# Kernel tuning notes

Measured on AMD Instinct MI355X. Metric: run time of the kernel, lower is better.

## Reference

```python
import jax, jax.numpy as jnp
import numpy as np

B, S, T = 256, 1024, 64  # batch, seq_len, num_tags


def setup_inputs() -> dict:
    key = jax.random.key(0)
    k1, k2, k3 = jax.random.split(key, 3)
    emissions = jax.random.normal(k1, (B, S, T), dtype=jnp.float32)
    tags = jax.random.randint(k2, (B, S), 0, T)
    mask = jnp.ones((B, S), dtype=bool)
    # nn.init.normal_(transitions, mean=0, std=0.1)
    transitions = 0.1 * jax.random.normal(k3, (T, T), dtype=jnp.float32)
    return {"emissions": emissions, "tags": tags, "mask": mask, "transitions": transitions}


def _crf_nll(emissions, transitions, tags, mask):
    maskf = mask.astype(emissions.dtype)
    # ---- gold score (_score_sentence) ----
    emit = jnp.take_along_axis(emissions, tags[..., None], axis=2)[..., 0]  # [B,S]
    emit_scores = (emit * maskf).sum(axis=1)
    trans_scores = (transitions[tags[:, :-1], tags[:, 1:]] * maskf[:, 1:]).sum(axis=1)
    gold = emit_scores + trans_scores  # [B]

    # ---- partition function (_forward_alg) via lax.scan ----
    alpha0 = emissions[:, 0]                      # [B,T]
    em_t = jnp.swapaxes(emissions[:, 1:], 0, 1)   # [S-1,B,T] time-major
    mk_t = jnp.swapaxes(mask[:, 1:], 0, 1)        # [S-1,B]

    def step(alpha, xs):
        e, m = xs
        # scores[b,i,j] = alpha[b,i] + trans[i,j] + emit[b,j]
        scores = alpha[:, :, None] + transitions[None, :, :] + e[:, None, :]
        new_alpha = jax.nn.logsumexp(scores, axis=1)  # [B,T]
        return jnp.where(m[:, None], new_alpha, alpha), None

    alpha, _ = jax.lax.scan(step, alpha0, (em_t, mk_t))
    fwd_score = jax.nn.logsumexp(alpha, axis=1)  # [B]

    # reduction='mean'
    return (fwd_score - gold).mean()


def reference(emissions, tags, mask, transitions):
    return _crf_nll(emissions, transitions, tags, mask)
```

## Files before the change

kernel.cpp:

```cpp
#include <hip/hip_runtime.h>
#include <hip/hip_bf16.h>
#include <cstdint>
#include <cstddef>


#define BB 256
#define SS 1024
#define TT 64
#define LN2f 0.69314718055994530942f

typedef _Float16 h2  __attribute__((ext_vector_type(2)));
typedef _Float16 h8  __attribute__((ext_vector_type(8)));
typedef float    f32x16 __attribute__((ext_vector_type(16)));
typedef int      i4v __attribute__((ext_vector_type(4)));

__device__ __forceinline__ float wred(float v) {
#pragma unroll
    for (int m = 32; m; m >>= 1) v += __shfl_xor(v, m, 64);
    return v;
}

__device__ __forceinline__ float rescale(float qn, int& kacc) {
    int bq = __builtin_amdgcn_readfirstlane(__float_as_int(qn));
    int k  = ((bq >> 23) & 255) - 127;
    kacc += k;
    return qn * __int_as_float((127 - k) << 23);
}

__device__ __forceinline__ float matvec64(float bc, const h2* Epk) {
    int nq = __builtin_amdgcn_mov_dpp(__float_as_int(bc), 0xB1, 0xF, 0xF, true);
    int pki = __builtin_bit_cast(int,
                  __builtin_amdgcn_cvt_pkrtz(bc, __int_as_float(nq)));
    int sp[32];
#pragma unroll
    for (int p = 0; p < 32; ++p)
        sp[p] = __builtin_amdgcn_readlane(pki, 2 * p);
    float a0 = 0.f, a1 = 0.f, a2 = 0.f, a3 = 0.f;
#pragma unroll
    for (int p = 0; p < 32; p += 4) {
        a0 = __builtin_amdgcn_fdot2(__builtin_bit_cast(h2, sp[p + 0]), Epk[p + 0], a0, false);
        a1 = __builtin_amdgcn_fdot2(__builtin_bit_cast(h2, sp[p + 1]), Epk[p + 1], a1, false);
        a2 = __builtin_amdgcn_fdot2(__builtin_bit_cast(h2, sp[p + 2]), Epk[p + 2], a2, false);
        a3 = __builtin_amdgcn_fdot2(__builtin_bit_cast(h2, sp[p + 3]), Epk[p + 3], a3, false);
    }
    return (a0 + a1) + (a2 + a3);
}

#define VSTEPF(EVAL)                                                       \
    {                                                                      \
        float ee = __expf(EVAL);                                           \
        float t  = matvec64(state, Epk);                                   \
        state    = rescale(t * ee, kacc);                                  \
    }
#define VSTEPB(EVAL)                                                       \
    {                                                                      \
        float ee = __expf(EVAL);                                           \
        float t  = matvec64(state * ee, Epk);                              \
        state    = rescale(t, kacc);                                       \
    }

#define PKRTZ(a, b) __builtin_bit_cast(int, __builtin_amdgcn_cvt_pkrtz((a), (b)))
#define SWAP32(x, y) asm("v_permlane32_swap_b32 %0, %1" : "+v"(x), "+v"(y))

#define CONV(CC, OUTA, OUTB)                                               \
    {                                                                      \
        int p0 = PKRTZ(CC[0], CC[1]);   int p1 = PKRTZ(CC[2], CC[3]);      \
        int p2 = PKRTZ(CC[4], CC[5]);   int p3 = PKRTZ(CC[6], CC[7]);      \
        SWAP32(p0, p2);  SWAP32(p1, p3);                                   \
        i4v da = {p0, p1, p2, p3};                                         \
        OUTA = __builtin_bit_cast(h8, da);                                 \
        int q0 = PKRTZ(CC[8], CC[9]);   int q1 = PKRTZ(CC[10], CC[11]);    \
        int q2 = PKRTZ(CC[12], CC[13]); int q3 = PKRTZ(CC[14], CC[15]);    \
        SWAP32(q0, q2);  SWAP32(q1, q3);                                   \
        i4v db = {q0, q1, q2, q3};                                         \
        OUTB = __builtin_bit_cast(h8, db);                                 \
    }

__device__ __forceinline__ f32x16 zz16() {
    f32x16 z;
#pragma unroll
    for (int q = 0; q < 16; ++q) z[q] = 0.f;
    return z;
}

#define MSTEP(E0V, E1V)                                                    \
    {                                                                      \
        float ee0 = __expf(E0V), ee1 = __expf(E1V);                        \
        float m0f = ee0 * minv, m1f = ee1 * minv;                          \
        h2 mp0 = __builtin_bit_cast(h2, __builtin_amdgcn_cvt_pkrtz(m0f, m0f)); \
        h2 mp1 = __builtin_bit_cast(h2, __builtin_amdgcn_cvt_pkrtz(m1f, m1f)); \
        h8 ms0 = __builtin_shufflevector(mp0, mp0, 0,1,0,1,0,1,0,1);       \
        h8 ms1 = __builtin_shufflevector(mp1, mp1, 0,1,0,1,0,1,0,1);       \
        h8 A0[4], A1[4];                                                   \
        _Pragma("unroll")                                                  \
        for (int kk = 0; kk < 4; ++kk) { A0[kk] = EfT[0][kk] * ms0;        \
                                         A1[kk] = EfT[1][kk] * ms1; }      \
        f32x16 c00 = zz16(), c01 = zz16(), c10 = zz16(), c11 = zz16();     \
        _Pragma("unroll")                                                  \
        for (int kk = 0; kk < 4; ++kk) {                                   \
            c00 = __builtin_amdgcn_mfma_f32_32x32x16_f16(A0[kk], Mb[0][kk], c00, 0, 0, 0); \
            c01 = __builtin_amdgcn_mfma_f32_32x32x16_f16(A0[kk], Mb[1][kk], c01, 0, 0, 0); \
            c10 = __builtin_amdgcn_mfma_f32_32x32x16_f16(A1[kk], Mb[0][kk], c10, 0, 0, 0); \
            c11 = __builtin_amdgcn_mfma_f32_32x32x16_f16(A1[kk], Mb[1][kk], c11, 0, 0, 0); \
        }                                                                  \
        int bq = __builtin_amdgcn_readfirstlane(__float_as_int(c00[0]));   \
        int k  = ((bq >> 23) & 255) - 127;                                 \
        kacc += k;                                                         \
        minv = __int_as_float((127 - k) << 23);                            \
        CONV(c00, Mb[0][0], Mb[0][1]);                                     \
        CONV(c10, Mb[0][2], Mb[0][3]);                                     \
        CONV(c01, Mb[1][0], Mb[1][1]);                                     \
        CONV(c11, Mb[1][2], Mb[1][3]);                                     \
    }

__device__ __forceinline__ void gold_gather(const float* __restrict__ em,
                                            const float* __restrict__ trans,
                                            const int* t0v, const int* t1v,
                                            int w, int j,
                                            float* ge, float* gt) {
#pragma unroll
    for (int c = 0; c < 4; ++c) {
        int s = (w * 4 + c) * TT + j;
        ge[c] = em[s * TT + t0v[c]];
        float tr = trans[t0v[c] * TT + t1v[c]];
        gt[c] = (s == SS - 1) ? 0.f : tr;
    }
}

__global__ __launch_bounds__(256) void crf_fwd_kernel(
    const float* __restrict__ emissions,
    const int*   __restrict__ tags,
    const float* __restrict__ trans,
    float*       __restrict__ ws)
{
    const int b   = blockIdx.x;
    const int tid = threadIdx.x;
    const int w   = tid >> 6;
    const int j   = tid & 63;
    const float* em = emissions + (size_t)b * (SS * TT);
    const int*   tg = tags + b * SS;

    __shared__ float shq[TT];
    __shared__ float shr[TT];
    __shared__ float shu[TT];
    __shared__ float shM[2][TT][65];
    __shared__ float shg[4];
    __shared__ int   shk_[4];

    int t0v[4], t1v[4];
#pragma unroll
    for (int c = 0; c < 4; ++c) {
        int s = (w * 4 + c) * TT + j;
        t0v[c] = tg[s];
        t1v[c] = tg[(s < SS - 1) ? s + 1 : s];
    }

    float ge[4], gt[4];
    int   kacc = 0;

    if (w < 2) {
        h2 Epk[32];
        float state;
        if (w == 0) {
#pragma unroll
            for (int p = 0; p < 32; ++p) {
                float x = __expf(trans[(2 * p + 0) * TT + j]);
                float y = __expf(trans[(2 * p + 1) * TT + j]);
                Epk[p] = __builtin_bit_cast(h2, __builtin_amdgcn_cvt_pkrtz(x, y));
            }
            state = __expf(em[j]);
            float eb[8];
#pragma unroll
            for (int u = 0; u < 8; ++u) eb[u] = em[(1 + u) * TT + j];
            gold_gather(em, trans, t0v, t1v, w, j, ge, gt);
            for (int s0 = 1; s0 < 264; s0 += 8) {
                float en[8];
#pragma unroll
                for (int u = 0; u < 8; ++u)
                    en[u] = em[(s0 + 8 + u) * TT + j];
#pragma unroll
                for (int u = 0; u < 8; ++u) VSTEPF(eb[u]);
#pragma unroll
                for (int u = 0; u < 8; ++u) eb[u] = en[u];
            }
            shq[j] = state;
        } else {
#pragma unroll
            for (int p = 0; p < 32; ++p) {
                float x = __expf(trans[j * TT + 2 * p + 0]);
                float y = __expf(trans[j * TT + 2 * p + 1]);
                Epk[p] = __builtin_bit_cast(h2, __builtin_amdgcn_cvt_pkrtz(x, y));
            }
            state = 1.0f;
            float ep[7], eb[8];
#pragma unroll
            for (int u = 0; u < 7; ++u) ep[u] = em[(1023 - u) * TT + j];
#pragma unroll
            for (int u = 0; u < 8; ++u) eb[u] = em[(1016 - u) * TT + j];
            gold_gather(em, trans, t0v, t1v, w, j, ge, gt);
#pragma unroll
            for (int u = 0; u < 7; ++u) VSTEPB(ep[u]);
            for (int t0 = 0; t0 < 256; t0 += 8) {
                float en[8];
#pragma unroll
                for (int u = 0; u < 8; ++u)
                    en[u] = em[(1016 - (t0 + 8 + u)) * TT + j];
#pragma unroll
                for (int u = 0; u < 8; ++u) VSTEPB(eb[u]);
#pragma unroll
                for (int u = 0; u < 8; ++u) eb[u] = en[u];
            }
            shr[j] = state;
        }
    } else {
        const int hh  = j >> 5;
        const int cc_ = j & 31;
        const int sbeg = (w == 2) ? 265 : 513;

        h8 EfT[2][4];
#pragma unroll
        for (int rr = 0; rr < 2; ++rr)
#pragma unroll
            for (int kk = 0; kk < 4; ++kk) {
                h8 v;
#pragma unroll
                for (int e = 0; e < 8; ++e)
                    v[e] = (_Float16)__expf(trans[(16 * kk + 8 * hh + e) * TT + 32 * rr + cc_]);
                EfT[rr][kk] = v;
            }
        h8 Mb[2][4];
#pragma unroll
        for (int gg = 0; gg < 2; ++gg)
#pragma unroll
            for (int kk = 0; kk < 4; ++kk) {
                h8 v;
#pragma unroll
                for (int e = 0; e < 8; ++e)
                    v[e] = (_Float16)((16 * kk + 8 * hh + e == 32 * gg + cc_) ? 1.0f : 0.0f);
                Mb[gg][kk] = v;
            }

        float minv = 1.0f;
        float eb0[4], eb1[4];
#pragma unroll
        for (int u = 0; u < 4; ++u) {
            eb0[u] = em[(sbeg + u) * TT + cc_];
            eb1[u] = em[(sbeg + u) * TT + 32 + cc_];
        }
        gold_gather(em, trans, t0v, t1v, w, j, ge, gt);

        for (int s0 = 0; s0 < 248; s0 += 4) {
            float en0[4], en1[4];
#pragma unroll
            for (int u = 0; u < 4; ++u) {
                en0[u] = em[(sbeg + s0 + 4 + u) * TT + cc_];
                en1[u] = em[(sbeg + s0 + 4 + u) * TT + 32 + cc_];
            }
#pragma unroll
            for (int u = 0; u < 4; ++u) MSTEP(eb0[u], eb1[u]);
#pragma unroll
            for (int u = 0; u < 4; ++u) { eb0[u] = en0[u]; eb1[u] = en1[u]; }
        }

        float* shMp = &shM[w - 2][0][0];
#pragma unroll
        for (int gg = 0; gg < 2; ++gg)
#pragma unroll
            for (int kk = 0; kk < 4; ++kk)
#pragma unroll
                for (int e = 0; e < 8; ++e)
                    shMp[(16 * kk + 8 * hh + e) * 65 + 32 * gg + cc_] =
                        (float)Mb[gg][kk][e] * minv;
    }

    float g = 0.f;
#pragma unroll
    for (int c = 0; c < 4; ++c) g += ge[c] + gt[c];
    g = wred(g);
    if (j == 0) { shg[w] = g; shk_[w] = kacc; }
    __syncthreads();

    if (w == 0) {
        float u_ = 0.f;
#pragma unroll 8
        for (int i = 0; i < TT; ++i) u_ += shq[i] * shM[0][j][i];
        shu[j] = u_;
        float y = 0.f;
#pragma unroll 8
        for (int i = 0; i < TT; ++i) y += shu[i] * shM[1][j][i];
        float pr  = y * shr[j];
        float sum = wred(pr);
        float fwd = __logf(sum) +
                    (float)(shk_[0] + shk_[1] + shk_[2] + shk_[3]) * LN2f;
        if (j == 0) ws[b] = fwd - (shg[0] + shg[1] + shg[2] + shg[3]);
    }
}

__global__ __launch_bounds__(256) void crf_reduce_kernel(
    const float* __restrict__ ws, float* __restrict__ out)
{
    int t = threadIdx.x;
    float v = ws[t];
#pragma unroll
    for (int m = 32; m; m >>= 1) v += __shfl_xor(v, m, 64);
    __shared__ float sh[4];
    if ((t & 63) == 0) sh[t >> 6] = v;
    __syncthreads();
    if (t == 0) out[0] = (sh[0] + sh[1] + sh[2] + sh[3]) * (1.0f / BB);
}

extern "C" void kernel_launch(void* const* d_in, const int* in_sizes, int n_in,
                              void* d_out, int out_size, void* d_ws, size_t ws_size,
                              hipStream_t stream) {
    const float* emissions = (const float*)d_in[0];
    const int*   tags      = (const int*)d_in[1];
    const float* trans     = (const float*)d_in[3];
    float* ws = (float*)d_ws;

    crf_fwd_kernel<<<BB, 256, 0, stream>>>(emissions, tags, trans, ws);
    crf_reduce_kernel<<<1, BB, 0, stream>>>(ws, (float*)d_out);
}
```

Before: 205.5 us.

## Split CRF sequence scan across six waves with four MFMA matrix segments

Raises the block from four waves to six. The two vector waves now scan longer forward and backward segments, and four MFMA waves each build a transfer-matrix product over a shorter 108-step middle chunk, so the serial dependency chain per wave gets shorter. Segment matrices are stored in fp16 shared memory without the last rescale factor. The combine step chains four matrix-vector products instead of two. The first MFMA of each step now takes a zero constant directly instead of a zeroed accumulator. Risks include more registers per block, lower occupancy, extra serial combine work and fp16 precision loss in the stored matrices.

```diff
diff --git a/kernel.cpp b/kernel.cpp
--- a/kernel.cpp
+++ b/kernel.cpp
@@ -8,6 +8,10 @@
 #define SS 1024
 #define TT 64
 #define LN2f 0.69314718055994530942f
+#define VF 296
+#define VB 295
+#define MM 108
+#define SB1 297
 
 typedef _Float16 h2  __attribute__((ext_vector_type(2)));
 typedef _Float16 h8  __attribute__((ext_vector_type(8)));
@@ -95,9 +99,12 @@
         _Pragma("unroll")                                                  \
         for (int kk = 0; kk < 4; ++kk) { A0[kk] = EfT[0][kk] * ms0;        \
                                          A1[kk] = EfT[1][kk] * ms1; }      \
-        f32x16 c00 = zz16(), c01 = zz16(), c10 = zz16(), c11 = zz16();     \
+        f32x16 c00 = __builtin_amdgcn_mfma_f32_32x32x16_f16(A0[0], Mb[0][0], CZ, 0, 0, 0); \
+        f32x16 c01 = __builtin_amdgcn_mfma_f32_32x32x16_f16(A0[0], Mb[1][0], CZ, 0, 0, 0); \
+        f32x16 c10 = __builtin_amdgcn_mfma_f32_32x32x16_f16(A1[0], Mb[0][0], CZ, 0, 0, 0); \
+        f32x16 c11 = __builtin_amdgcn_mfma_f32_32x32x16_f16(A1[0], Mb[1][0], CZ, 0, 0, 0); \
         _Pragma("unroll")                                                  \
-        for (int kk = 0; kk < 4; ++kk) {                                   \
+        for (int kk = 1; kk < 4; ++kk) {                                   \
             c00 = __builtin_amdgcn_mfma_f32_32x32x16_f16(A0[kk], Mb[0][kk], c00, 0, 0, 0); \
             c01 = __builtin_amdgcn_mfma_f32_32x32x16_f16(A0[kk], Mb[1][kk], c01, 0, 0, 0); \
             c10 = __builtin_amdgcn_mfma_f32_32x32x16_f16(A1[kk], Mb[0][kk], c10, 0, 0, 0); \
@@ -105,7 +112,7 @@
         }                                                                  \
         int bq = __builtin_amdgcn_readfirstlane(__float_as_int(c00[0]));   \
         int k  = ((bq >> 23) & 255) - 127;                                 \
-        kacc += k;                                                         \
+        kacc += k;  klast = k;                                             \
         minv = __int_as_float((127 - k) << 23);                            \
         CONV(c00, Mb[0][0], Mb[0][1]);                                     \
         CONV(c10, Mb[0][2], Mb[0][3]);                                     \
@@ -116,18 +123,18 @@
 __device__ __forceinline__ void gold_gather(const float* __restrict__ em,
                                             const float* __restrict__ trans,
                                             const int* t0v, const int* t1v,
-                                            int w, int j,
+                                            int qw, int j,
                                             float* ge, float* gt) {
 #pragma unroll
     for (int c = 0; c < 4; ++c) {
-        int s = (w * 4 + c) * TT + j;
+        int s = (qw * 4 + c) * TT + j;
         ge[c] = em[s * TT + t0v[c]];
         float tr = trans[t0v[c] * TT + t1v[c]];
         gt[c] = (s == SS - 1) ? 0.f : tr;
     }
 }
 
-__global__ __launch_bounds__(256) void crf_fwd_kernel(
+__global__ __launch_bounds__(384) void crf_fwd_kernel(
     const float* __restrict__ emissions,
     const int*   __restrict__ tags,
     const float* __restrict__ trans,
@@ -140,82 +147,86 @@
     const float* em = emissions + (size_t)b * (SS * TT);
     const int*   tg = tags + b * SS;
 
-    __shared__ float shq[TT];
-    __shared__ float shr[TT];
-    __shared__ float shu[TT];
-    __shared__ float shM[2][TT][65];
-    __shared__ float shg[4];
-    __shared__ int   shk_[4];
+    __shared__ float     shq[TT];
+    __shared__ float     shr[TT];
+    __shared__ float     shu[TT];
+    __shared__ _Float16  shM[4][TT][66];
+    __shared__ float     shg[6];
+    __shared__ int       shk_[6];
 
     int t0v[4], t1v[4];
-#pragma unroll
-    for (int c = 0; c < 4; ++c) {
-        int s = (w * 4 + c) * TT + j;
-        t0v[c] = tg[s];
-        t1v[c] = tg[(s < SS - 1) ? s + 1 : s];
-    }
-
-    float ge[4], gt[4];
+    if (w < 4) {
+#pragma unroll
+        for (int c = 0; c < 4; ++c) {
+            int s = (w * 4 + c) * TT + j;
+            t0v[c] = tg[s];
+            t1v[c] = tg[(s < SS - 1) ? s + 1 : s];
+        }
+    }
+
+    float ge[4] = {0.f, 0.f, 0.f, 0.f}, gt[4] = {0.f, 0.f, 0.f, 0.f};
     int   kacc = 0;
-
-    if (w < 2) {
+    int   krep = 0;
+
+    if (w == 2) {
         h2 Epk[32];
-        float state;
-        if (w == 0) {
-#pragma unroll
-            for (int p = 0; p < 32; ++p) {
-                float x = __expf(trans[(2 * p + 0) * TT + j]);
-                float y = __expf(trans[(2 * p + 1) * TT + j]);
-                Epk[p] = __builtin_bit_cast(h2, __builtin_amdgcn_cvt_pkrtz(x, y));
-            }
-            state = __expf(em[j]);
-            float eb[8];
-#pragma unroll
-            for (int u = 0; u < 8; ++u) eb[u] = em[(1 + u) * TT + j];
-            gold_gather(em, trans, t0v, t1v, w, j, ge, gt);
-            for (int s0 = 1; s0 < 264; s0 += 8) {
-                float en[8];
-#pragma unroll
-                for (int u = 0; u < 8; ++u)
-                    en[u] = em[(s0 + 8 + u) * TT + j];
-#pragma unroll
-                for (int u = 0; u < 8; ++u) VSTEPF(eb[u]);
-#pragma unroll
-                for (int u = 0; u < 8; ++u) eb[u] = en[u];
-            }
-            shq[j] = state;
-        } else {
-#pragma unroll
-            for (int p = 0; p < 32; ++p) {
-                float x = __expf(trans[j * TT + 2 * p + 0]);
-                float y = __expf(trans[j * TT + 2 * p + 1]);
-                Epk[p] = __builtin_bit_cast(h2, __builtin_amdgcn_cvt_pkrtz(x, y));
-            }
-            state = 1.0f;
-            float ep[7], eb[8];
-#pragma unroll
-            for (int u = 0; u < 7; ++u) ep[u] = em[(1023 - u) * TT + j];
-#pragma unroll
-            for (int u = 0; u < 8; ++u) eb[u] = em[(1016 - u) * TT + j];
-            gold_gather(em, trans, t0v, t1v, w, j, ge, gt);
-#pragma unroll
-            for (int u = 0; u < 7; ++u) VSTEPB(ep[u]);
-            for (int t0 = 0; t0 < 256; t0 += 8) {
-                float en[8];
-#pragma unroll
-                for (int u = 0; u < 8; ++u)
-                    en[u] = em[(1016 - (t0 + 8 + u)) * TT + j];
-#pragma unroll
-                for (int u = 0; u < 8; ++u) VSTEPB(eb[u]);
-#pragma unroll
-                for (int u = 0; u < 8; ++u) eb[u] = en[u];
-            }
-            shr[j] = state;
-        }
+#pragma unroll
+        for (int p = 0; p < 32; ++p) {
+            float x = __expf(trans[(2 * p + 0) * TT + j]);
+            float y = __expf(trans[(2 * p + 1) * TT + j]);
+            Epk[p] = __builtin_bit_cast(h2, __builtin_amdgcn_cvt_pkrtz(x, y));
+        }
+        float state = __expf(em[j]);
+        float eb[8];
+#pragma unroll
+        for (int u = 0; u < 8; ++u) eb[u] = em[(1 + u) * TT + j];
+        gold_gather(em, trans, t0v, t1v, w, j, ge, gt);
+        for (int s0 = 1; s0 < 1 + VF; s0 += 8) {
+            float en[8];
+#pragma unroll
+            for (int u = 0; u < 8; ++u)
+                en[u] = em[(s0 + 8 + u) * TT + j];
+#pragma unroll
+            for (int u = 0; u < 8; ++u) VSTEPF(eb[u]);
+#pragma unroll
+            for (int u = 0; u < 8; ++u) eb[u] = en[u];
+        }
+        shq[j] = state;
+        krep = kacc;
+    } else if (w == 3) {
+        h2 Epk[32];
+#pragma unroll
+        for (int p = 0; p < 32; ++p) {
+            float x = __expf(trans[j * TT + 2 * p + 0]);
+            float y = __expf(trans[j * TT + 2 * p + 1]);
+            Epk[p] = __builtin_bit_cast(h2, __builtin_amdgcn_cvt_pkrtz(x, y));
+        }
+        float state = 1.0f;
+        float ep[7], eb[8];
+#pragma unroll
+        for (int u = 0; u < 7; ++u) ep[u] = em[(1023 - u) * TT + j];
+#pragma unroll
+        for (int u = 0; u < 8; ++u) eb[u] = em[(1016 - u) * TT + j];
+        gold_gather(em, trans, t0v, t1v, w, j, ge, gt);
+#pragma unroll
+        for (int u = 0; u < 7; ++u) VSTEPB(ep[u]);
+        for (int t0 = 0; t0 < 288; t0 += 8) {
+            float en[8];
+#pragma unroll
+            for (int u = 0; u < 8; ++u)
+                en[u] = em[(1016 - (t0 + 8 + u)) * TT + j];
+#pragma unroll
+            for (int u = 0; u < 8; ++u) VSTEPB(eb[u]);
+#pragma unroll
+            for (int u = 0; u < 8; ++u) eb[u] = en[u];
+        }
+        shr[j] = state;
+        krep = kacc;
     } else {
-        const int hh  = j >> 5;
-        const int cc_ = j & 31;
-        const int sbeg = (w == 2) ? 265 : 513;
+        const int mi   = (w < 2) ? w : (w - 2);
+        const int sbeg = SB1 + MM * mi;
+        const int hh   = j >> 5;
+        const int cc_  = j & 31;
 
         h8 EfT[2][4];
 #pragma unroll
@@ -240,16 +251,18 @@
                 Mb[gg][kk] = v;
             }
 
+        const f32x16 CZ = zz16();
         float minv = 1.0f;
+        int   klast = 0;
         float eb0[4], eb1[4];
 #pragma unroll
         for (int u = 0; u < 4; ++u) {
             eb0[u] = em[(sbeg + u) * TT + cc_];
             eb1[u] = em[(sbeg + u) * TT + 32 + cc_];
         }
-        gold_gather(em, trans, t0v, t1v, w, j, ge, gt);
-
-        for (int s0 = 0; s0 < 248; s0 += 4) {
+        if (w < 4) gold_gather(em, trans, t0v, t1v, w, j, ge, gt);
+
+        for (int s0 = 0; s0 < MM; s0 += 4) {
             float en0[4], en1[4];
 #pragma unroll
             for (int u = 0; u < 4; ++u) {
@@ -262,37 +275,41 @@
             for (int u = 0; u < 4; ++u) { eb0[u] = en0[u]; eb1[u] = en1[u]; }
         }
 
-        float* shMp = &shM[w - 2][0][0];
 #pragma unroll
         for (int gg = 0; gg < 2; ++gg)
 #pragma unroll
             for (int kk = 0; kk < 4; ++kk)
 #pragma unroll
                 for (int e = 0; e < 8; ++e)
-                    shMp[(16 * kk + 8 * hh + e) * 65 + 32 * gg + cc_] =
-                        (float)Mb[gg][kk][e] * minv;
+                    shM[mi][16 * kk + 8 * hh + e][32 * gg + cc_] = Mb[gg][kk][e];
+        krep = kacc - klast;
     }
 
     float g = 0.f;
 #pragma unroll
     for (int c = 0; c < 4; ++c) g += ge[c] + gt[c];
     g = wred(g);
-    if (j == 0) { shg[w] = g; shk_[w] = kacc; }
+    if (j == 0) { shg[w] = g; shk_[w] = krep; }
     __syncthreads();
 
-    if (w == 0) {
-        float u_ = 0.f;
+    if (w == 2) {
+        float uv = 0.f;
 #pragma unroll 8
-        for (int i = 0; i < TT; ++i) u_ += shq[i] * shM[0][j][i];
-        shu[j] = u_;
-        float y = 0.f;
+        for (int i = 0; i < TT; ++i) uv += shq[i] * (float)shM[0][j][i];
+#pragma unroll 1
+        for (int m = 1; m < 4; ++m) {
+            shu[j] = uv;
+            float acc = 0.f;
 #pragma unroll 8
-        for (int i = 0; i < TT; ++i) y += shu[i] * shM[1][j][i];
-        float pr  = y * shr[j];
+            for (int i = 0; i < TT; ++i) acc += shu[i] * (float)shM[m][j][i];
+            uv = acc;
+        }
+        float pr  = uv * shr[j];
         float sum = wred(pr);
-        float fwd = __logf(sum) +
-                    (float)(shk_[0] + shk_[1] + shk_[2] + shk_[3]) * LN2f;
-        if (j == 0) ws[b] = fwd - (shg[0] + shg[1] + shg[2] + shg[3]);
+        int ksum = shk_[0] + shk_[1] + shk_[2] + shk_[3] + shk_[4] + shk_[5];
+        float fwd = __logf(sum) + (float)ksum * LN2f;
+        float gsum = shg[0] + shg[1] + shg[2] + shg[3] + shg[4] + shg[5];
+        if (j == 0) ws[b] = fwd - gsum;
     }
 }
 
@@ -317,6 +334,6 @@
     const float* trans     = (const float*)d_in[3];
     float* ws = (float*)d_ws;
 
-    crf_fwd_kernel<<<BB, 256, 0, stream>>>(emissions, tags, trans, ws);
+    crf_fwd_kernel<<<BB, 384, 0, stream>>>(emissions, tags, trans, ws);
     crf_reduce_kernel<<<1, BB, 0, stream>>>(ws, (float*)d_out);
 }
```

After: 165.8 us. -19.3%, faster.

## Split CRF sequence across six waves with interleaved matrix chains and backward matrix-vector combine

Applied to the files above, without the earlier changes.

Each block grows from four to six waves. Two waves now run the forward and backward vector recurrences over about 272 steps each. Four MFMA waves each run two independent 60-step transfer-matrix chains, interleaved so their latencies overlap. The matrix products are applied to the backward vector in sequence, with exponent rescaling, through shared memory instead of storing full fp32 matrices. The gold-score gather moves onto the vector waves. This shortens the serial critical path per sequence at the cost of more waves per block, more registers, and eight synchronized combine steps at the end.

```diff
diff --git a/kernel.cpp b/kernel.cpp
--- a/kernel.cpp
+++ b/kernel.cpp
@@ -8,6 +8,10 @@
 #define SS 1024
 #define TT 64
 #define LN2f 0.69314718055994530942f
+#define VF 272
+#define VB 271
+#define MMs 60
+#define MSB 273
 
 typedef _Float16 h2  __attribute__((ext_vector_type(2)));
 typedef _Float16 h8  __attribute__((ext_vector_type(8)));
@@ -83,10 +87,10 @@
     return z;
 }
 
-#define MSTEP(E0V, E1V)                                                    \
+#define MSTEP(MB, MINV, KACC, KLAST, E0V, E1V)                             \
     {                                                                      \
         float ee0 = __expf(E0V), ee1 = __expf(E1V);                        \
-        float m0f = ee0 * minv, m1f = ee1 * minv;                          \
+        float m0f = ee0 * MINV, m1f = ee1 * MINV;                          \
         h2 mp0 = __builtin_bit_cast(h2, __builtin_amdgcn_cvt_pkrtz(m0f, m0f)); \
         h2 mp1 = __builtin_bit_cast(h2, __builtin_amdgcn_cvt_pkrtz(m1f, m1f)); \
         h8 ms0 = __builtin_shufflevector(mp0, mp0, 0,1,0,1,0,1,0,1);       \
@@ -95,39 +99,28 @@
         _Pragma("unroll")                                                  \
         for (int kk = 0; kk < 4; ++kk) { A0[kk] = EfT[0][kk] * ms0;        \
                                          A1[kk] = EfT[1][kk] * ms1; }      \
-        f32x16 c00 = zz16(), c01 = zz16(), c10 = zz16(), c11 = zz16();     \
+        f32x16 c00 = __builtin_amdgcn_mfma_f32_32x32x16_f16(A0[0], MB[0][0], CZ, 0, 0, 0); \
+        f32x16 c01 = __builtin_amdgcn_mfma_f32_32x32x16_f16(A0[0], MB[1][0], CZ, 0, 0, 0); \
+        f32x16 c10 = __builtin_amdgcn_mfma_f32_32x32x16_f16(A1[0], MB[0][0], CZ, 0, 0, 0); \
+        f32x16 c11 = __builtin_amdgcn_mfma_f32_32x32x16_f16(A1[0], MB[1][0], CZ, 0, 0, 0); \
         _Pragma("unroll")                                                  \
-        for (int kk = 0; kk < 4; ++kk) {                                   \
-            c00 = __builtin_amdgcn_mfma_f32_32x32x16_f16(A0[kk], Mb[0][kk], c00, 0, 0, 0); \
-            c01 = __builtin_amdgcn_mfma_f32_32x32x16_f16(A0[kk], Mb[1][kk], c01, 0, 0, 0); \
-            c10 = __builtin_amdgcn_mfma_f32_32x32x16_f16(A1[kk], Mb[0][kk], c10, 0, 0, 0); \
-            c11 = __builtin_amdgcn_mfma_f32_32x32x16_f16(A1[kk], Mb[1][kk], c11, 0, 0, 0); \
+        for (int kk = 1; kk < 4; ++kk) {                                   \
+            c00 = __builtin_amdgcn_mfma_f32_32x32x16_f16(A0[kk], MB[0][kk], c00, 0, 0, 0); \
+            c01 = __builtin_amdgcn_mfma_f32_32x32x16_f16(A0[kk], MB[1][kk], c01, 0, 0, 0); \
+            c10 = __builtin_amdgcn_mfma_f32_32x32x16_f16(A1[kk], MB[0][kk], c10, 0, 0, 0); \
+            c11 = __builtin_amdgcn_mfma_f32_32x32x16_f16(A1[kk], MB[1][kk], c11, 0, 0, 0); \
         }                                                                  \
         int bq = __builtin_amdgcn_readfirstlane(__float_as_int(c00[0]));   \
         int k  = ((bq >> 23) & 255) - 127;                                 \
-        kacc += k;                                                         \
-        minv = __int_as_float((127 - k) << 23);                            \
-        CONV(c00, Mb[0][0], Mb[0][1]);                                     \
-        CONV(c10, Mb[0][2], Mb[0][3]);                                     \
-        CONV(c01, Mb[1][0], Mb[1][1]);                                     \
-        CONV(c11, Mb[1][2], Mb[1][3]);                                     \
-    }
-
-__device__ __forceinline__ void gold_gather(const float* __restrict__ em,
-                                            const float* __restrict__ trans,
-                                            const int* t0v, const int* t1v,
-                                            int w, int j,
-                                            float* ge, float* gt) {
-#pragma unroll
-    for (int c = 0; c < 4; ++c) {
-        int s = (w * 4 + c) * TT + j;
-        ge[c] = em[s * TT + t0v[c]];
-        float tr = trans[t0v[c] * TT + t1v[c]];
-        gt[c] = (s == SS - 1) ? 0.f : tr;
-    }
-}
-
-__global__ __launch_bounds__(256) void crf_fwd_kernel(
+        KACC += k;  KLAST = k;                                             \
+        MINV = __int_as_float((127 - k) << 23);                            \
+        CONV(c00, MB[0][0], MB[0][1]);                                     \
+        CONV(c10, MB[0][2], MB[0][3]);                                     \
+        CONV(c01, MB[1][0], MB[1][1]);                                     \
+        CONV(c11, MB[1][2], MB[1][3]);                                     \
+    }
+
+__global__ __launch_bounds__(384) void crf_fwd_kernel(
     const float* __restrict__ emissions,
     const int*   __restrict__ tags,
     const float* __restrict__ trans,
@@ -141,27 +134,35 @@
     const int*   tg = tags + b * SS;
 
     __shared__ float shq[TT];
-    __shared__ float shr[TT];
     __shared__ float shu[TT];
-    __shared__ float shM[2][TT][65];
-    __shared__ float shg[4];
-    __shared__ int   shk_[4];
-
-    int t0v[4], t1v[4];
-#pragma unroll
-    for (int c = 0; c < 4; ++c) {
-        int s = (w * 4 + c) * TT + j;
-        t0v[c] = tg[s];
-        t1v[c] = tg[(s < SS - 1) ? s + 1 : s];
-    }
-
-    float ge[4], gt[4];
-    int   kacc = 0;
-
-    if (w < 2) {
+    __shared__ float shg[2];
+    __shared__ int   shkk[10];
+    __shared__ int   shkr;
+
+    if (tid == 0) shkr = 0;
+
+    const bool isMat = (w == 0) || (w == 1) || (w == 4) || (w == 5);
+    const int  widx  = (w < 2) ? w : (w - 2);
+    const int  hh    = j >> 5;
+    const int  cc_   = j & 31;
+
+    h8 MbA[2][4], MbB[2][4];
+
+    if (w == 2 || w == 3) {
+        int t0v[8], t1v[8];
+#pragma unroll
+        for (int c = 0; c < 8; ++c) {
+            int s = ((w - 2) * 8 + c) * TT + j;
+            t0v[c] = tg[s];
+            t1v[c] = tg[(s < SS - 1) ? s + 1 : s];
+        }
+
         h2 Epk[32];
         float state;
-        if (w == 0) {
+        int  kacc = 0;
+        float ge[8], gt[8];
+
+        if (w == 2) {
 #pragma unroll
             for (int p = 0; p < 32; ++p) {
                 float x = __expf(trans[(2 * p + 0) * TT + j]);
@@ -172,8 +173,13 @@
             float eb[8];
 #pragma unroll
             for (int u = 0; u < 8; ++u) eb[u] = em[(1 + u) * TT + j];
-            gold_gather(em, trans, t0v, t1v, w, j, ge, gt);
-            for (int s0 = 1; s0 < 264; s0 += 8) {
+#pragma unroll
+            for (int c = 0; c < 8; ++c) {
+                int s = (0 * 8 + c) * TT + j;
+                ge[c] = em[s * TT + t0v[c]];
+                gt[c] = trans[t0v[c] * TT + t1v[c]];
+            }
+            for (int s0 = 1; s0 < 1 + VF; s0 += 8) {
                 float en[8];
 #pragma unroll
                 for (int u = 0; u < 8; ++u)
@@ -197,10 +203,16 @@
             for (int u = 0; u < 7; ++u) ep[u] = em[(1023 - u) * TT + j];
 #pragma unroll
             for (int u = 0; u < 8; ++u) eb[u] = em[(1016 - u) * TT + j];
-            gold_gather(em, trans, t0v, t1v, w, j, ge, gt);
+#pragma unroll
+            for (int c = 0; c < 8; ++c) {
+                int s = (8 + c) * TT + j;
+                ge[c] = em[s * TT + t0v[c]];
+                float tr = trans[t0v[c] * TT + t1v[c]];
+                gt[c] = (s == SS - 1) ? 0.f : tr;
+            }
 #pragma unroll
             for (int u = 0; u < 7; ++u) VSTEPB(ep[u]);
-            for (int t0 = 0; t0 < 256; t0 += 8) {
+            for (int t0 = 0; t0 < VB - 7; t0 += 8) {
                 float en[8];
 #pragma unroll
                 for (int u = 0; u < 8; ++u)
@@ -210,12 +222,17 @@
 #pragma unroll
                 for (int u = 0; u < 8; ++u) eb[u] = en[u];
             }
-            shr[j] = state;
-        }
+            shu[j] = state;
+        }
+
+        float g = 0.f;
+#pragma unroll
+        for (int c = 0; c < 8; ++c) g += ge[c] + gt[c];
+        g = wred(g);
+        if (j == 0) { shg[w - 2] = g; shkk[8 + (w - 2)] = kacc; }
     } else {
-        const int hh  = j >> 5;
-        const int cc_ = j & 31;
-        const int sbeg = (w == 2) ? 265 : 513;
+        const int sA = MSB + MMs * (2 * widx);
+        const int sB = sA + MMs;
 
         h8 EfT[2][4];
 #pragma unroll
@@ -228,7 +245,6 @@
                     v[e] = (_Float16)__expf(trans[(16 * kk + 8 * hh + e) * TT + 32 * rr + cc_]);
                 EfT[rr][kk] = v;
             }
-        h8 Mb[2][4];
 #pragma unroll
         for (int gg = 0; gg < 2; ++gg)
 #pragma unroll
@@ -237,62 +253,85 @@
 #pragma unroll
                 for (int e = 0; e < 8; ++e)
                     v[e] = (_Float16)((16 * kk + 8 * hh + e == 32 * gg + cc_) ? 1.0f : 0.0f);
-                Mb[gg][kk] = v;
-            }
-
-        float minv = 1.0f;
-        float eb0[4], eb1[4];
+                MbA[gg][kk] = v;
+                MbB[gg][kk] = v;
+            }
+
+        const f32x16 CZ = zz16();
+        float minvA = 1.0f, minvB = 1.0f;
+        int   kaccA = 0, kaccB = 0, klastA = 0, klastB = 0;
+        float ebA0[4], ebA1[4], ebB0[4], ebB1[4];
 #pragma unroll
         for (int u = 0; u < 4; ++u) {
-            eb0[u] = em[(sbeg + u) * TT + cc_];
-            eb1[u] = em[(sbeg + u) * TT + 32 + cc_];
-        }
-        gold_gather(em, trans, t0v, t1v, w, j, ge, gt);
-
-        for (int s0 = 0; s0 < 248; s0 += 4) {
-            float en0[4], en1[4];
+            ebA0[u] = em[(sA + u) * TT + cc_];
+            ebA1[u] = em[(sA + u) * TT + 32 + cc_];
+            ebB0[u] = em[(sB + u) * TT + cc_];
+            ebB1[u] = em[(sB + u) * TT + 32 + cc_];
+        }
+
+        for (int s0 = 0; s0 < MMs; s0 += 4) {
+            float enA0[4], enA1[4], enB0[4], enB1[4];
 #pragma unroll
             for (int u = 0; u < 4; ++u) {
-                en0[u] = em[(sbeg + s0 + 4 + u) * TT + cc_];
-                en1[u] = em[(sbeg + s0 + 4 + u) * TT + 32 + cc_];
-            }
-#pragma unroll
-            for (int u = 0; u < 4; ++u) MSTEP(eb0[u], eb1[u]);
-#pragma unroll
-            for (int u = 0; u < 4; ++u) { eb0[u] = en0[u]; eb1[u] = en1[u]; }
-        }
-
-        float* shMp = &shM[w - 2][0][0];
-#pragma unroll
-        for (int gg = 0; gg < 2; ++gg)
+                enA0[u] = em[(sA + s0 + 4 + u) * TT + cc_];
+                enA1[u] = em[(sA + s0 + 4 + u) * TT + 32 + cc_];
+                enB0[u] = em[(sB + s0 + 4 + u) * TT + cc_];
+                enB1[u] = em[(sB + s0 + 4 + u) * TT + 32 + cc_];
+            }
+#pragma unroll
+            for (int u = 0; u < 4; ++u) {
+                MSTEP(MbA, minvA, kaccA, klastA, ebA0[u], ebA1[u]);
+                MSTEP(MbB, minvB, kaccB, klastB, ebB0[u], ebB1[u]);
+            }
+#pragma unroll
+            for (int u = 0; u < 4; ++u) {
+                ebA0[u] = enA0[u]; ebA1[u] = enA1[u];
+                ebB0[u] = enB0[u]; ebB1[u] = enB1[u];
+            }
+        }
+        if (j == 0) {
+            shkk[2 * widx]     = kaccA - klastA;
+            shkk[2 * widx + 1] = kaccB - klastB;
+        }
+    }
+
+    __syncthreads();
+
+#pragma unroll
+    for (int m = 7; m >= 0; --m) {
+        if (isMat && (m >> 1) == widx) {
+            const bool useB = (m & 1) != 0;
+            float p0 = 0.f, p1 = 0.f;
 #pragma unroll
             for (int kk = 0; kk < 4; ++kk)
 #pragma unroll
-                for (int e = 0; e < 8; ++e)
-                    shMp[(16 * kk + 8 * hh + e) * 65 + 32 * gg + cc_] =
-                        (float)Mb[gg][kk][e] * minv;
-    }
-
-    float g = 0.f;
-#pragma unroll
-    for (int c = 0; c < 4; ++c) g += ge[c] + gt[c];
-    g = wred(g);
-    if (j == 0) { shg[w] = g; shk_[w] = kacc; }
-    __syncthreads();
-
-    if (w == 0) {
-        float u_ = 0.f;
-#pragma unroll 8
-        for (int i = 0; i < TT; ++i) u_ += shq[i] * shM[0][j][i];
-        shu[j] = u_;
-        float y = 0.f;
-#pragma unroll 8
-        for (int i = 0; i < TT; ++i) y += shu[i] * shM[1][j][i];
-        float pr  = y * shr[j];
+                for (int e = 0; e < 8; ++e) {
+                    float uval = shu[16 * kk + 8 * hh + e];
+                    _Float16 a0 = useB ? MbB[0][kk][e] : MbA[0][kk][e];
+                    _Float16 a1 = useB ? MbB[1][kk][e] : MbA[1][kk][e];
+                    p0 += (float)a0 * uval;
+                    p1 += (float)a1 * uval;
+                }
+            p0 += __shfl_xor(p0, 32, 64);
+            p1 += __shfl_xor(p1, 32, 64);
+            int bu = __builtin_amdgcn_readfirstlane(__float_as_int(p0));
+            int ku = ((bu >> 23) & 255) - 127;
+            float sc = __int_as_float((127 - ku) << 23);
+            shu[cc_]      = p0 * sc;
+            shu[32 + cc_] = p1 * sc;
+            if (j == 0) shkr += ku;
+        }
+        __syncthreads();
+    }
+
+    if (w == 2) {
+        float pr  = shq[j] * shu[j];
         float sum = wred(pr);
-        float fwd = __logf(sum) +
-                    (float)(shk_[0] + shk_[1] + shk_[2] + shk_[3]) * LN2f;
-        if (j == 0) ws[b] = fwd - (shg[0] + shg[1] + shg[2] + shg[3]);
+        int ksum = shkr;
+#pragma unroll
+        for (int q = 0; q < 10; ++q) ksum += shkk[q];
+        float fwd = __logf(sum) + (float)ksum * LN2f;
+        if (j == 0) ws[b] = fwd - (shg[0] + shg[1]);
     }
 }
 
@@ -317,6 +356,6 @@
     const float* trans     = (const float*)d_in[3];
     float* ws = (float*)d_ws;
 
-    crf_fwd_kernel<<<BB, 256, 0, stream>>>(emissions, tags, trans, ws);
+    crf_fwd_kernel<<<BB, 384, 0, stream>>>(emissions, tags, trans, ws);
     crf_reduce_kernel<<<1, BB, 0, stream>>>(ws, (float*)d_out);
 }
```

Result: faster. 176.1 us (-14.3%).
